# Performance work log

Hardware: AMD Instinct MI355X
Metric: run time of the kernel (lower is better)

The kernel has to match this reference:

```python
import jax, jax.numpy as jnp
import numpy as np

IMG_W = 512.0
IMG_H = 512.0
LOC_VARIANCE = (0.1, 0.1, 0.2, 0.2)
IOU_THRESHOLD = 0.5
SCORE_THRESHOLD = 0.02
MAX_DETECTIONS = 100
NUM_ANCHORS = 200000
NUM_CLASSES = 91  # includes background class 0


def setup_inputs() -> dict:
    key = jax.random.key(0)
    k1, k2, k3 = jax.random.split(key, 3)
    predictions = jax.random.normal(k1, (1, NUM_ANCHORS, 4 + NUM_CLASSES), dtype=jnp.float32)
    # default boxes in (cx, cy, w, h), roughly inside a 512x512 image
    cxy = jax.random.uniform(k2, (NUM_ANCHORS, 2), dtype=jnp.float32) * IMG_W
    wh = jax.random.uniform(k3, (NUM_ANCHORS, 2), dtype=jnp.float32) * 96.0 + 8.0
    default_boxes = jnp.concatenate([cxy, wh], axis=-1)
    return {"predictions": predictions, "default_boxes": default_boxes}


def _greedy_nms(boxes, scores_work, max_det, iou_thr):
    # boxes: [N,4] corners; scores_work: [N] with invalid entries = -inf
    n = boxes.shape[0]
    areas = (boxes[:, 2] - boxes[:, 0]) * (boxes[:, 3] - boxes[:, 1])
    arange_n = jnp.arange(n)

    def body(i, state):
        sw, idxs, valid = state
        j = jnp.argmax(sw)
        ok = sw[j] > -jnp.inf
        box = boxes[j]
        lt = jnp.maximum(box[:2], boxes[:, :2])
        rb = jnp.minimum(box[2:], boxes[:, 2:])
        whd = jnp.clip(rb - lt, 0.0, None)
        inter = whd[:, 0] * whd[:, 1]
        iou = inter / (areas[j] + areas - inter + 1e-9)
        suppress = (iou > iou_thr) | (arange_n == j)
        sw = jnp.where(ok & suppress, -jnp.inf, sw)
        idxs = idxs.at[i].set(jnp.where(ok, j, 0))
        valid = valid.at[i].set(ok)
        return sw, idxs, valid

    idxs0 = jnp.zeros((max_det,), dtype=jnp.int32)
    valid0 = jnp.zeros((max_det,), dtype=bool)
    _, idxs, valid = jax.lax.fori_loop(0, max_det, body, (scores_work, idxs0, valid0))
    return idxs, valid


def reference(predictions, default_boxes):
    preds = predictions[0]  # [N, 4 + C]
    var = jnp.asarray(LOC_VARIANCE, dtype=preds.dtype)
    loc = preds[:, :4] * var
    cls = jax.nn.softmax(preds[:, 4:], axis=-1)

    # decode cxcywh
    cxy = loc[:, :2] * default_boxes[:, 2:] + default_boxes[:, :2]
    wh = jnp.exp(loc[:, 2:]) * default_boxes[:, 2:]
    corners = jnp.concatenate([cxy - 0.5 * wh, cxy + 0.5 * wh], axis=-1)
    lims = jnp.asarray([IMG_W, IMG_H, IMG_W, IMG_H], dtype=corners.dtype)
    boxes = jnp.clip(corners, 0.0, lims)  # [N,4] x1,y1,x2,y2

    cls_ids = jnp.argmax(cls, axis=-1)
    cls_scores = jnp.max(cls, axis=-1)

    # background filter + score threshold, expressed as masking (fixed shapes)
    fg = cls_ids != 0
    scores_work = jnp.where(fg & (cls_scores >= SCORE_THRESHOLD), cls_scores, -jnp.inf)

    nms_idx, valid = _greedy_nms(boxes, scores_work, MAX_DETECTIONS, IOU_THRESHOLD)

    dec_boxes = jnp.where(valid[:, None], boxes[nms_idx], 0.0)
    dec_ids = jnp.where(valid, cls_ids[nms_idx] - 1, -1)
    dec_scores = jnp.where(valid, cls_scores[nms_idx], 0.0)
    return dec_boxes, dec_ids, dec_scores
```

## Files before the change

### kernel.cpp

```cpp
#include <hip/hip_runtime.h>
#include <stdint.h>

#define N_ANCHORS   200000
#define NUM_CLASSES 91
#define PRED_STRIDE 95
#define TILE_BYTES  24320
#define MAX_DET     100
#define CAP         4096
#define M_TARGET    3600
#define NBUCKETS    65536
#define NREP        8
#define N_TILES     3125

__device__ __forceinline__ void gload_lds16(const void* g, void* l) {
  __builtin_amdgcn_global_load_lds(
      (const __attribute__((address_space(1))) uint32_t*)g,
      (__attribute__((address_space(3))) uint32_t*)l, 16, 0, 0);
}

__device__ __forceinline__ unsigned long long umax64(unsigned long long a,
                                                     unsigned long long b) {
  return a > b ? a : b;
}
__device__ __forceinline__ unsigned long long umin64(unsigned long long a,
                                                     unsigned long long b) {
  return a < b ? a : b;
}
__device__ __forceinline__ void cex(unsigned long long& a, unsigned long long& b,
                                    bool up) {
  unsigned long long mx = a > b ? a : b;
  unsigned long long mn = a > b ? b : a;
  a = up ? mx : mn;
  b = up ? mn : mx;
}

__global__ __launch_bounds__(256) void zero_kernel(unsigned int* __restrict__ hist,
                                                   int* __restrict__ ctr) {
  int i = blockIdx.x * 256 + threadIdx.x;
  if (i < NREP * NBUCKETS) hist[i] = 0u;
  if (i == 0) ctr[0] = 0;
}

__global__ __launch_bounds__(128) void decode_kernel(
    const float* __restrict__ pred, const float* __restrict__ dbx,
    float4* __restrict__ boxes, unsigned long long* __restrict__ keys,
    unsigned int* __restrict__ hist)
{
  __shared__ float tile[2][64 * PRED_STRIDE];
  const int wv   = threadIdx.x >> 6;
  const int lane = threadIdx.x & 63;
  const int w    = blockIdx.x * 2 + wv;
  if (w >= N_TILES) return;
  float* T = tile[wv];
  const char* src = (const char*)pred + (size_t)w * TILE_BYTES;

#pragma unroll
  for (int q = 0; q < 23; ++q)
    gload_lds16(src + q * 1024 + lane * 16, &T[q * 256]);
  gload_lds16(src + 23296 + lane * 16, &T[5824]);
  asm volatile("s_waitcnt vmcnt(0)" ::: "memory");
  __builtin_amdgcn_sched_barrier(0);

  const float* R = T + lane * PRED_STRIDE;

  float m = R[4]; int am = 0;
#pragma unroll
  for (int j = 1; j < NUM_CLASSES; ++j) {
    float v = R[4 + j];
    if (v > m) { m = v; am = j; }
  }
  float s = 0.f;
#pragma unroll
  for (int j = 0; j < NUM_CLASSES; ++j) s += expf(R[4 + j] - m);
  float score = 1.0f / s;

  const int gi = w * 64 + lane;
  float4 d = ((const float4*)dbx)[gi];
  float lx = R[0] * 0.1f, ly = R[1] * 0.1f, lw = R[2] * 0.2f, lh = R[3] * 0.2f;
  float cx = lx * d.z + d.x;
  float cy = ly * d.w + d.y;
  float bw = expf(lw) * d.z;
  float bh = expf(lh) * d.w;
  float x1 = fminf(fmaxf(cx - 0.5f * bw, 0.f), 512.f);
  float y1 = fminf(fmaxf(cy - 0.5f * bh, 0.f), 512.f);
  float x2 = fminf(fmaxf(cx + 0.5f * bw, 0.f), 512.f);
  float y2 = fminf(fmaxf(cy + 0.5f * bh, 0.f), 512.f);
  boxes[gi] = make_float4(x1, y1, x2, y2);

  bool valid = (am != 0) && (score >= 0.02f);
  unsigned int sb = __float_as_uint(score);
  unsigned int payload = ~(((unsigned int)gi << 7) | (unsigned int)am);
  unsigned long long key = valid ? (((unsigned long long)sb << 32) | payload) : 0ull;
  keys[gi] = key;
  if (valid) atomicAdd(&hist[(w & (NREP - 1)) * NBUCKETS + (sb >> 16)], 1u);
}

__global__ __launch_bounds__(256) void chunksum_kernel(
    const unsigned int* __restrict__ hist, unsigned int* __restrict__ chunksum)
{
  int tid = blockIdx.x * 256 + threadIdx.x;
  int W = tid >> 6, lane = tid & 63;
  unsigned int s = 0;
#pragma unroll
  for (int r = 0; r < NREP; ++r) s += hist[r * NBUCKETS + W * 64 + lane];
  for (int off = 32; off; off >>= 1) s += __shfl_down(s, off);
  if (lane == 0) chunksum[W] = s;
}

__global__ __launch_bounds__(1024) void thresh_kernel(
    const unsigned int* __restrict__ hist, const unsigned int* __restrict__ chunksum,
    unsigned int* __restrict__ thr)
{
  __shared__ unsigned int csum[1024];
  __shared__ unsigned int cbuf[64];
  __shared__ int cstar;
  __shared__ unsigned int cafter;
  int t = threadIdx.x;
  csum[t] = chunksum[t];
  if (t == 0) cstar = -1;
  __syncthreads();
  for (int off = 1; off < 1024; off <<= 1) {
    unsigned int v = (t + off < 1024) ? csum[t + off] : 0u;
    __syncthreads();
    csum[t] += v;
    __syncthreads();
  }
  unsigned int mine  = csum[t];
  unsigned int after = (t == 1023) ? 0u : csum[t + 1];
  if (mine >= M_TARGET && (t == 1023 || after < M_TARGET)) {
    cstar = t; cafter = after;
  }
  if (t == 0 && csum[0] < M_TARGET) thr[0] = 0u;
  __syncthreads();
  if (t < 64 && cstar >= 0) {
    int b = cstar * 64 + t;
    unsigned int cnt = 0;
#pragma unroll
    for (int r = 0; r < NREP; ++r) cnt += hist[r * NBUCKETS + b];
    cbuf[t] = cnt;
  }
  __syncthreads();
  if (t == 0 && cstar >= 0) {
    unsigned int running = cafter;
    unsigned int thrv = 0u;
    for (int i = 63; i >= 0; --i) {
      running += cbuf[i];
      if (running >= M_TARGET) {
        unsigned int b = (unsigned int)(cstar * 64 + i);
        thrv = (running > CAP) ? ((b + 1) << 16) : (b << 16);
        break;
      }
    }
    thr[0] = thrv;
  }
}

__global__ __launch_bounds__(256) void compact_kernel(
    const unsigned long long* __restrict__ keys, const unsigned int* __restrict__ thr,
    unsigned long long* __restrict__ cand, int* __restrict__ ctr)
{
  int i = blockIdx.x * 256 + threadIdx.x;
  if (i >= N_ANCHORS) return;
  unsigned long long k = keys[i];
  if (k != 0ull) {
    unsigned int sb = (unsigned int)(k >> 32);
    if (sb >= thr[0]) {
      int pos = atomicAdd(ctr, 1);
      if (pos < CAP) cand[pos] = k;
    }
  }
}

__global__ __launch_bounds__(1024) void nms_kernel(
    const unsigned long long* __restrict__ cand, const int* __restrict__ ctr,
    const float4* __restrict__ boxes, float* __restrict__ out)
{
  __shared__ unsigned long long sk[CAP];
  __shared__ float4 abox[MAX_DET];
  __shared__ float aarea[MAX_DET];
  __shared__ unsigned long long akey[MAX_DET];
  __shared__ int acount;

  const int t = threadIdx.x;
  int K = ctr[0]; if (K > CAP) K = CAP;

  unsigned long long r0, r1, r2, r3;
  {
    const int b = 4 * t;
    r0 = (b + 0 < K) ? cand[b + 0] : 0ull;
    r1 = (b + 1 < K) ? cand[b + 1] : 0ull;
    r2 = (b + 2 < K) ? cand[b + 2] : 0ull;
    r3 = (b + 3 < K) ? cand[b + 3] : 0ull;
  }

  for (int k = 2; k <= CAP; k <<= 1) {
    for (int j = k >> 1; j > 0; j >>= 1) {
      const bool up = (((4 * t) & k) == 0);
      if (j >= 256) {
        sk[4 * t + 0] = r0; sk[4 * t + 1] = r1;
        sk[4 * t + 2] = r2; sk[4 * t + 3] = r3;
        __syncthreads();
        const int pt = 4 * (t ^ (j >> 2));
        unsigned long long p0 = sk[pt + 0], p1 = sk[pt + 1];
        unsigned long long p2 = sk[pt + 2], p3 = sk[pt + 3];
        const bool takemax = (up == ((t & (j >> 2)) == 0));
        r0 = takemax ? umax64(r0, p0) : umin64(r0, p0);
        r1 = takemax ? umax64(r1, p1) : umin64(r1, p1);
        r2 = takemax ? umax64(r2, p2) : umin64(r2, p2);
        r3 = takemax ? umax64(r3, p3) : umin64(r3, p3);
        __syncthreads();
      } else if (j >= 4) {
        const int lx = j >> 2;
        const bool takemax = (up == ((t & lx) == 0));
        unsigned long long p;
        p = __shfl_xor(r0, lx); r0 = takemax ? umax64(r0, p) : umin64(r0, p);
        p = __shfl_xor(r1, lx); r1 = takemax ? umax64(r1, p) : umin64(r1, p);
        p = __shfl_xor(r2, lx); r2 = takemax ? umax64(r2, p) : umin64(r2, p);
        p = __shfl_xor(r3, lx); r3 = takemax ? umax64(r3, p) : umin64(r3, p);
      } else if (j == 2) {
        cex(r0, r2, up); cex(r1, r3, up);
      } else {
        if (k == 2) { cex(r0, r1, true); cex(r2, r3, false); }
        else        { cex(r0, r1, up);   cex(r2, r3, up);   }
      }
    }
  }
  sk[4 * t + 0] = r0; sk[4 * t + 1] = r1;
  sk[4 * t + 2] = r2; sk[4 * t + 3] = r3;
  __syncthreads();

  if (threadIdx.x < 64) {
    int lane = threadIdx.x;
    int ac = 0;
    for (int gbase = 0; gbase < CAP && ac < MAX_DET; gbase += 64) {
      if (gbase >= K) break;
      __asm__ __volatile__("" ::: "memory");
      unsigned long long key = sk[gbase + lane];
      bool alive = (key != 0ull);
      float4 b = make_float4(0.f, 0.f, 0.f, 0.f);
      float area = 0.f;
      if (alive) {
        unsigned int pay = ~(unsigned int)key;
        int idx = (int)(pay >> 7);
        b = boxes[idx];
        area = (b.z - b.x) * (b.w - b.y);
      }
      for (int a2 = 0; a2 < ac; ++a2) {
        if (alive) {
          float4 ab = abox[a2];
          float lx = fmaxf(ab.x, b.x), ly = fmaxf(ab.y, b.y);
          float rx = fminf(ab.z, b.z), ry = fminf(ab.w, b.w);
          float iw = fmaxf(rx - lx, 0.f), ih = fmaxf(ry - ly, 0.f);
          float inter = iw * ih;
          float iou = inter / (aarea[a2] + area - inter + 1e-9f);
          if (iou > 0.5f) alive = false;
        }
      }
      while (ac < MAX_DET) {
        unsigned long long mv = __ballot(alive);
        if (mv == 0ull) break;
        int first = __ffsll(mv) - 1;
        float wx1 = __shfl(b.x, first), wy1 = __shfl(b.y, first);
        float wx2 = __shfl(b.z, first), wy2 = __shfl(b.w, first);
        float wa  = __shfl(area, first);
        if (lane == first) {
          abox[ac] = b; aarea[ac] = area; akey[ac] = key;
          alive = false;
        }
        __asm__ __volatile__("" ::: "memory");
        if (alive) {
          float lx = fmaxf(wx1, b.x), ly = fmaxf(wy1, b.y);
          float rx = fminf(wx2, b.z), ry = fminf(wy2, b.w);
          float iw = fmaxf(rx - lx, 0.f), ih = fmaxf(ry - ly, 0.f);
          float inter = iw * ih;
          float iou = inter / (wa + area - inter + 1e-9f);
          if (iou > 0.5f) alive = false;
        }
        ++ac;
      }
    }
    if (lane == 0) acount = ac;
  }
  __syncthreads();

  if (t < MAX_DET) {
    float bx1 = 0.f, by1 = 0.f, bx2 = 0.f, by2 = 0.f, idf = -1.f, sc = 0.f;
    if (t < acount) {
      unsigned long long key = akey[t];
      float4 b = abox[t];
      bx1 = b.x; by1 = b.y; bx2 = b.z; by2 = b.w;
      unsigned int pay = ~(unsigned int)key;
      int clsid = (int)(pay & 0x7Fu);
      idf = (float)(clsid - 1);
      sc = __uint_as_float((unsigned int)(key >> 32));
    }
    out[t * 4 + 0] = bx1; out[t * 4 + 1] = by1;
    out[t * 4 + 2] = bx2; out[t * 4 + 3] = by2;
    out[400 + t] = idf;
    out[500 + t] = sc;
  }
}

extern "C" void kernel_launch(void* const* d_in, const int* in_sizes, int n_in,
                              void* d_out, int out_size, void* d_ws, size_t ws_size,
                              hipStream_t stream) {
  (void)in_sizes; (void)n_in; (void)out_size; (void)ws_size;
  const float* pred = (const float*)d_in[0];
  const float* dbx  = (const float*)d_in[1];
  float* out = (float*)d_out;

  char* ws = (char*)d_ws;
  float4*             boxes = (float4*)(ws);
  unsigned long long* keys  = (unsigned long long*)(ws + 3200000);
  unsigned int*       hist  = (unsigned int*)(ws + 4800000);
  unsigned int*       csums = (unsigned int*)(ws + 6897152);
  int*                ctr   = (int*)(ws + 6901248);
  unsigned int*       thr   = (unsigned int*)(ws + 6901264);
  unsigned long long* cand  = (unsigned long long*)(ws + 6901280);

  hipLaunchKernelGGL(zero_kernel, dim3((NREP * NBUCKETS) / 256), dim3(256), 0, stream,
                     hist, ctr);
  hipLaunchKernelGGL(decode_kernel, dim3((N_TILES + 1) / 2), dim3(128), 0, stream,
                     pred, dbx, boxes, keys, hist);
  hipLaunchKernelGGL(chunksum_kernel, dim3(NBUCKETS / 256), dim3(256), 0, stream,
                     hist, csums);
  hipLaunchKernelGGL(thresh_kernel, dim3(1), dim3(1024), 0, stream,
                     hist, csums, thr);
  hipLaunchKernelGGL(compact_kernel, dim3((N_ANCHORS + 255) / 256), dim3(256), 0, stream,
                     keys, thr, cand, ctr);
  hipLaunchKernelGGL(nms_kernel, dim3(1), dim3(1024), 0, stream,
                     cand, ctr, boxes, out);
}
```

Before: 220.3 us.

## Split candidate sort into four parallel block sorts plus merge-path merges

```diff
diff --git a/kernel.cpp b/kernel.cpp
--- a/kernel.cpp
+++ b/kernel.cpp
@@ -7,6 +7,7 @@
 #define TILE_BYTES  24320
 #define MAX_DET     100
 #define CAP         4096
+#define CAPS        1024
 #define M_TARGET    3600
 #define NBUCKETS    65536
 #define NREP        8
@@ -32,6 +33,27 @@
   unsigned long long mn = a > b ? b : a;
   a = up ? mx : mn;
   b = up ? mn : mx;
+}
+
+__device__ __forceinline__ void merge8(
+    const unsigned long long* __restrict__ A, int nA,
+    const unsigned long long* __restrict__ B, int nB,
+    unsigned long long* __restrict__ C, int d)
+{
+  int lo = d - nB; if (lo < 0) lo = 0;
+  int hi = d < nA ? d : nA;
+  while (lo < hi) {
+    int mid = (lo + hi) >> 1;
+    if (A[mid] < B[d - 1 - mid]) hi = mid; else lo = mid + 1;
+  }
+  int i = lo, j = d - lo;
+#pragma unroll
+  for (int e = 0; e < 8; ++e) {
+    bool takeA = (j >= nB) || (i < nA && A[i] >= B[j]);
+    unsigned long long v = takeA ? A[i] : B[j];
+    C[d + e] = v;
+    if (takeA) ++i; else ++j;
+  }
 }
 
 __global__ __launch_bounds__(256) void zero_kernel(unsigned int* __restrict__ hist,
@@ -171,29 +193,24 @@
   }
 }
 
-__global__ __launch_bounds__(1024) void nms_kernel(
-    const unsigned long long* __restrict__ cand, const int* __restrict__ ctr,
-    const float4* __restrict__ boxes, float* __restrict__ out)
-{
-  __shared__ unsigned long long sk[CAP];
-  __shared__ float4 abox[MAX_DET];
-  __shared__ float aarea[MAX_DET];
-  __shared__ unsigned long long akey[MAX_DET];
-  __shared__ int acount;
-
+__global__ __launch_bounds__(256) void sort4_kernel(
+    unsigned long long* __restrict__ cand, const int* __restrict__ ctr)
+{
+  __shared__ unsigned long long sk[CAPS];
   const int t = threadIdx.x;
+  const int base = blockIdx.x * CAPS;
   int K = ctr[0]; if (K > CAP) K = CAP;
 
   unsigned long long r0, r1, r2, r3;
   {
-    const int b = 4 * t;
+    const int b = base + 4 * t;
     r0 = (b + 0 < K) ? cand[b + 0] : 0ull;
     r1 = (b + 1 < K) ? cand[b + 1] : 0ull;
     r2 = (b + 2 < K) ? cand[b + 2] : 0ull;
     r3 = (b + 3 < K) ? cand[b + 3] : 0ull;
   }
 
-  for (int k = 2; k <= CAP; k <<= 1) {
+  for (int k = 2; k <= CAPS; k <<= 1) {
     for (int j = k >> 1; j > 0; j >>= 1) {
       const bool up = (((4 * t) & k) == 0);
       if (j >= 256) {
@@ -225,8 +242,38 @@
       }
     }
   }
-  sk[4 * t + 0] = r0; sk[4 * t + 1] = r1;
-  sk[4 * t + 2] = r2; sk[4 * t + 3] = r3;
+  {
+    const int b = base + 4 * t;
+    cand[b + 0] = r0; cand[b + 1] = r1;
+    cand[b + 2] = r2; cand[b + 3] = r3;
+  }
+}
+
+__global__ __launch_bounds__(512) void nms_kernel(
+    const unsigned long long* __restrict__ cand, const int* __restrict__ ctr,
+    const float4* __restrict__ boxes, float* __restrict__ out)
+{
+  __shared__ unsigned long long ska[CAP];
+  __shared__ unsigned long long skb[CAP];
+  __shared__ float4 abox[MAX_DET];
+  __shared__ float aarea[MAX_DET];
+  __shared__ unsigned long long akey[MAX_DET];
+  __shared__ int acount;
+
+  const int t = threadIdx.x;
+  int K = ctr[0]; if (K > CAP) K = CAP;
+
+  for (int i = t; i < CAP; i += 512) ska[i] = cand[i];
+  __syncthreads();
+
+  {
+    const int half = t >> 8;
+    const int tt = t & 255;
+    merge8(&ska[half * 2048], CAPS, &ska[half * 2048 + CAPS], CAPS,
+           &skb[half * 2048], tt * 8);
+  }
+  __syncthreads();
+  merge8(&skb[0], 2048, &skb[2048], 2048, &ska[0], t * 8);
   __syncthreads();
 
   if (threadIdx.x < 64) {
@@ -235,7 +282,7 @@
     for (int gbase = 0; gbase < CAP && ac < MAX_DET; gbase += 64) {
       if (gbase >= K) break;
       __asm__ __volatile__("" ::: "memory");
-      unsigned long long key = sk[gbase + lane];
+      unsigned long long key = ska[gbase + lane];
       bool alive = (key != 0ull);
       float4 b = make_float4(0.f, 0.f, 0.f, 0.f);
       float area = 0.f;
@@ -328,6 +375,8 @@
                      hist, csums, thr);
   hipLaunchKernelGGL(compact_kernel, dim3((N_ANCHORS + 255) / 256), dim3(256), 0, stream,
                      keys, thr, cand, ctr);
-  hipLaunchKernelGGL(nms_kernel, dim3(1), dim3(1024), 0, stream,
+  hipLaunchKernelGGL(sort4_kernel, dim3(4), dim3(256), 0, stream,
+                     cand, ctr);
+  hipLaunchKernelGGL(nms_kernel, dim3(1), dim3(512), 0, stream,
                      cand, ctr, boxes, out);
 }
```

Measured after the change: 211.4 us. 4.0% less time.
